# Performance work log

Measured on AMD Instinct MI355X. Metric: run time of the kernel, lower is better.

Reference implementation:

```python
import jax, jax.numpy as jnp
import numpy as np


def setup_inputs() -> dict:
    key = jax.random.key(0)
    B, Tt, Ts, C = 8, 128, 128, 512
    x = jax.random.normal(key, (B, Tt, Ts, C), dtype=jnp.float32)
    return {"x": x}


def reference(x) -> jnp.ndarray:
    # Original: xpool[:, t, j, :] = max over x[:, t, :j+1, :] along Ts.
    # This is exactly a running (prefix) max along the Ts axis (axis=2);
    # the outer loop over t is independent per row.
    xpool = jax.lax.cummax(x, axis=2)  # [B, Tt, Ts, C]
    return xpool
```

## Files before the change

kernel.cpp:

```cpp
#include <hip/hip_runtime.h>


constexpr int TS     = 128;
constexpr int CV     = 128;
constexpr int CHUNK  = 16;
constexpr int NCHUNK = TS / CHUNK;

typedef float nativef4 __attribute__((ext_vector_type(4)));

__device__ __forceinline__ float4 fmax4(float4 a, float4 b) {
  return make_float4(fmaxf(a.x, b.x), fmaxf(a.y, b.y),
                     fmaxf(a.z, b.z), fmaxf(a.w, b.w));
}

__device__ __forceinline__ void nt_store(float4* dst, float4 v) {
  __builtin_nontemporal_store(*reinterpret_cast<nativef4*>(&v),
                              reinterpret_cast<nativef4*>(dst));
}

template <int CH>
__device__ __forceinline__ void load_chunk(float4 (&buf)[CHUNK],
                                           const float4* __restrict__ p) {
#pragma unroll
  for (int i = 0; i < CHUNK; ++i)
    buf[i] = p[(size_t)(CH * CHUNK + i) * CV];
}

template <int CH>
__device__ __forceinline__ void scan_store_chunk(float4 (&buf)[CHUNK],
                                                 float4& carry,
                                                 float4* __restrict__ q) {
  buf[0] = fmax4(buf[0], carry);
#pragma unroll
  for (int i = 1; i < CHUNK; ++i) buf[i] = fmax4(buf[i], buf[i - 1]);
#pragma unroll
  for (int i = 0; i < CHUNK; ++i)
    nt_store(&q[(size_t)(CH * CHUNK + i) * CV], buf[i]);
  carry = buf[CHUNK - 1];
}

__global__ __launch_bounds__(256, 2) void cummax_scan(
    const float4* __restrict__ x, float4* __restrict__ out) {
  const int tid  = threadIdx.x;
  const int wid  = tid >> 6;
  const int lane = tid & 63;
  const int task = (blockIdx.x << 2) | wid;
  const int row  = task >> 1;
  const int cv   = ((task & 1) << 6) | lane;

  const size_t base = (size_t)row * TS * CV + cv;
  const float4* __restrict__ p = x + base;
  float4*       __restrict__ q = out + base;

  const float ninf = -__builtin_inff();
  float4 carry = make_float4(ninf, ninf, ninf, ninf);

  float4 a[CHUNK], b[CHUNK];

  load_chunk<0>(a, p);
  load_chunk<1>(b, p);
  scan_store_chunk<0>(a, carry, q);
  load_chunk<2>(a, p);
  scan_store_chunk<1>(b, carry, q);
  load_chunk<3>(b, p);
  scan_store_chunk<2>(a, carry, q);
  load_chunk<4>(a, p);
  scan_store_chunk<3>(b, carry, q);
  load_chunk<5>(b, p);
  scan_store_chunk<4>(a, carry, q);
  load_chunk<6>(a, p);
  scan_store_chunk<5>(b, carry, q);
  load_chunk<7>(b, p);
  scan_store_chunk<6>(a, carry, q);
  scan_store_chunk<7>(b, carry, q);
}

extern "C" void kernel_launch(void* const* d_in, const int* in_sizes, int n_in,
                              void* d_out, int out_size, void* d_ws, size_t ws_size,
                              hipStream_t stream) {
  const float4* x = (const float4*)d_in[0];
  float4* out = (float4*)d_out;

  cummax_scan<<<512, 256, 0, stream>>>(x, out);
}
```

Before: 446.8 us.

## Split Ts scan across waves with shared-memory chunk totals for more parallelism

Replaces the one-wave-per-column serial scan with a block of 16 waves, each scanning an 8-element chunk of Ts. Chunk totals are exchanged through shared memory to compute carries. Loads are switched to nontemporal. This greatly increases the number of waves and outstanding memory requests to better saturate HBM bandwidth, at the cost of a block-wide barrier and a small serial carry loop.

```diff
diff --git a/kernel.cpp b/kernel.cpp
--- a/kernel.cpp
+++ b/kernel.cpp
@@ -3,8 +3,9 @@
 
 constexpr int TS     = 128;
 constexpr int CV     = 128;
-constexpr int CHUNK  = 16;
+constexpr int CHUNK  = 8;
 constexpr int NCHUNK = TS / CHUNK;
+constexpr int CVB    = 64;
 
 typedef float nativef4 __attribute__((ext_vector_type(4)));
 
@@ -13,66 +14,51 @@
                      fmaxf(a.z, b.z), fmaxf(a.w, b.w));
 }
 
+__device__ __forceinline__ float4 nt_load(const float4* src) {
+  nativef4 t = __builtin_nontemporal_load(
+      reinterpret_cast<const nativef4*>(src));
+  return *reinterpret_cast<float4*>(&t);
+}
+
 __device__ __forceinline__ void nt_store(float4* dst, float4 v) {
   __builtin_nontemporal_store(*reinterpret_cast<nativef4*>(&v),
                               reinterpret_cast<nativef4*>(dst));
 }
 
-template <int CH>
-__device__ __forceinline__ void load_chunk(float4 (&buf)[CHUNK],
-                                           const float4* __restrict__ p) {
-#pragma unroll
-  for (int i = 0; i < CHUNK; ++i)
-    buf[i] = p[(size_t)(CH * CHUNK + i) * CV];
-}
+__global__ __launch_bounds__(1024) void cummax_scan(
+    const float4* __restrict__ x, float4* __restrict__ out) {
+  __shared__ float4 totals[NCHUNK][CVB];
 
-template <int CH>
-__device__ __forceinline__ void scan_store_chunk(float4 (&buf)[CHUNK],
-                                                 float4& carry,
-                                                 float4* __restrict__ q) {
-  buf[0] = fmax4(buf[0], carry);
-#pragma unroll
-  for (int i = 1; i < CHUNK; ++i) buf[i] = fmax4(buf[i], buf[i - 1]);
-#pragma unroll
-  for (int i = 0; i < CHUNK; ++i)
-    nt_store(&q[(size_t)(CH * CHUNK + i) * CV], buf[i]);
-  carry = buf[CHUNK - 1];
-}
+  const int tid   = threadIdx.x;
+  const int chunk = tid >> 6;
+  const int cvl   = tid & 63;
+  const int row   = blockIdx.x >> 1;
+  const int cv    = ((blockIdx.x & 1) << 6) | cvl;
 
-__global__ __launch_bounds__(256, 2) void cummax_scan(
-    const float4* __restrict__ x, float4* __restrict__ out) {
-  const int tid  = threadIdx.x;
-  const int wid  = tid >> 6;
-  const int lane = tid & 63;
-  const int task = (blockIdx.x << 2) | wid;
-  const int row  = task >> 1;
-  const int cv   = ((task & 1) << 6) | lane;
-
-  const size_t base = (size_t)row * TS * CV + cv;
+  const size_t base = ((size_t)row * TS + (size_t)chunk * CHUNK) * CV + cv;
   const float4* __restrict__ p = x + base;
   float4*       __restrict__ q = out + base;
 
+  float4 v[CHUNK];
+#pragma unroll
+  for (int i = 0; i < CHUNK; ++i) v[i] = nt_load(p + (size_t)i * CV);
+
+#pragma unroll
+  for (int i = 1; i < CHUNK; ++i) v[i] = fmax4(v[i], v[i - 1]);
+
+  totals[chunk][cvl] = v[CHUNK - 1];
+  __syncthreads();
+
   const float ninf = -__builtin_inff();
   float4 carry = make_float4(ninf, ninf, ninf, ninf);
+  for (int c = 0; c < chunk; ++c) {
+    carry = fmax4(carry, totals[c][cvl]);
+  }
 
-  float4 a[CHUNK], b[CHUNK];
-
-  load_chunk<0>(a, p);
-  load_chunk<1>(b, p);
-  scan_store_chunk<0>(a, carry, q);
-  load_chunk<2>(a, p);
-  scan_store_chunk<1>(b, carry, q);
-  load_chunk<3>(b, p);
-  scan_store_chunk<2>(a, carry, q);
-  load_chunk<4>(a, p);
-  scan_store_chunk<3>(b, carry, q);
-  load_chunk<5>(b, p);
-  scan_store_chunk<4>(a, carry, q);
-  load_chunk<6>(a, p);
-  scan_store_chunk<5>(b, carry, q);
-  load_chunk<7>(b, p);
-  scan_store_chunk<6>(a, carry, q);
-  scan_store_chunk<7>(b, carry, q);
+#pragma unroll
+  for (int i = 0; i < CHUNK; ++i) {
+    nt_store(q + (size_t)i * CV, fmax4(carry, v[i]));
+  }
 }
 
 extern "C" void kernel_launch(void* const* d_in, const int* in_sizes, int n_in,
@@ -81,5 +67,6 @@
   const float4* x = (const float4*)d_in[0];
   float4* out = (float4*)d_out;
 
-  cummax_scan<<<512, 256, 0, stream>>>(x, out);
+  constexpr int ROWS = 8 * 128;
+  cummax_scan<<<ROWS * 2, 1024, 0, stream>>>(x, out);
 }
```

Measured after the change: 417.2 us. 1.07x faster.
